# Performance work log

Measured on AMD Instinct MI355X. Metric: run time of the kernel, lower is better.

The kernel has to match this reference:

```python
import jax, jax.numpy as jnp
import numpy as np

B, H0, W0, C, NH, G = 2, 256, 256, 64, 4, 8
PD = (C // 4) // 4  # DynamicPosBias pos_dim = 4
HID = 4 * C


def _ln(x, g, b, eps=1e-5):
    mu = jnp.mean(x, -1, keepdims=True)
    var = jnp.mean((x - mu) ** 2, -1, keepdims=True)
    return (x - mu) * jax.lax.rsqrt(var + eps) * g + b


def setup_inputs():
    key = jax.random.key(0)
    ks = iter(jax.random.split(key, 48))
    w = lambda shape: jax.random.normal(next(ks), shape, jnp.float32) * 0.02
    return {
        'x': jax.random.normal(next(ks), (B, H0 * W0, C), jnp.float32),
        'y': jax.random.normal(next(ks), (B, H0 * W0, C), jnp.float32),
        'norm1_g': jnp.ones((C,), jnp.float32), 'norm1_b': jnp.zeros((C,), jnp.float32),
        'qkv_w': w((C, 3 * C)), 'qkv_b': jnp.zeros((3 * C,), jnp.float32),
        'proj_w': w((C, C)), 'proj_b': jnp.zeros((C,), jnp.float32),
        'pp_w': w((2, PD)), 'pp_b': jnp.zeros((PD,), jnp.float32),
        'ln1_g': jnp.ones((PD,), jnp.float32), 'ln1_b': jnp.zeros((PD,), jnp.float32),
        'l1_w': w((PD, PD)), 'l1_b': jnp.zeros((PD,), jnp.float32),
        'ln2_g': jnp.ones((PD,), jnp.float32), 'ln2_b': jnp.zeros((PD,), jnp.float32),
        'l2_w': w((PD, PD)), 'l2_b': jnp.zeros((PD,), jnp.float32),
        'ln3_g': jnp.ones((PD,), jnp.float32), 'ln3_b': jnp.zeros((PD,), jnp.float32),
        'l3_w': w((PD, NH)), 'l3_b': jnp.zeros((NH,), jnp.float32),
        'norm2_g': jnp.ones((C,), jnp.float32), 'norm2_b': jnp.zeros((C,), jnp.float32),
        'fx1_w': w((C, HID)), 'fx1_b': jnp.zeros((HID,), jnp.float32),
        'fx2_w': w((HID, C)), 'fx2_b': jnp.zeros((C,), jnp.float32),
        'fy1_w': w((C, HID)), 'fy1_b': jnp.zeros((HID,), jnp.float32),
        'fy2_w': w((HID, C)), 'fy2_b': jnp.zeros((C,), jnp.float32),
        'H': H0, 'W': W0,
    }


def reference(x, y, norm1_g, norm1_b, qkv_w, qkv_b, proj_w, proj_b,
              pp_w, pp_b, ln1_g, ln1_b, l1_w, l1_b, ln2_g, ln2_b, l2_w, l2_b,
              ln3_g, ln3_b, l3_w, l3_b, norm2_g, norm2_b,
              fx1_w, fx1_b, fx2_w, fx2_b, fy1_w, fy1_b, fy2_w, fy2_b, H, W):
    Bb, L, Cc = x.shape
    d = Cc // NH
    xn = _ln(x, norm1_g, norm1_b).reshape(Bb, H, W, Cc)
    yn = _ln(y, norm1_g, norm1_b).reshape(Bb, H, W, Cc)

    def part(t):  # (B,H,W,C) -> (B*nW, G*G, C)
        t = t.reshape(Bb, H // G, G, W // G, G, Cc).transpose(0, 1, 3, 2, 4, 5)
        return t.reshape(-1, G * G, Cc)

    # merge both modalities' patches of the same window along the token axis
    tok = tok = jnp.concatenate([part(xn), part(yn)], axis=1)  # (B_, 2*G*G, C)
    Gh, Gw = 2 * G, G
    N = Gh * Gw

    # dynamic relative position bias (small MLP + gather)
    bh = jnp.arange(1 - Gh, Gh)
    bw = jnp.arange(1 - Gw, Gw)
    biases = jnp.stack(jnp.meshgrid(bh, bw, indexing='ij'), 0).reshape(2, -1).T.astype(x.dtype)
    coords = jnp.stack(jnp.meshgrid(jnp.arange(Gh), jnp.arange(Gw), indexing='ij'), 0).reshape(2, -1)
    rel = (coords[:, :, None] - coords[:, None, :]).transpose(1, 2, 0)
    ridx = (rel[..., 0] + Gh - 1) * (2 * Gw - 1) + (rel[..., 1] + Gw - 1)  # (N,N)
    p = biases @ pp_w + pp_b
    p = jax.nn.relu(_ln(p, ln1_g, ln1_b)) @ l1_w + l1_b
    p = jax.nn.relu(_ln(p, ln2_g, ln2_b)) @ l2_w + l2_b
    p = jax.nn.relu(_ln(p, ln3_g, ln3_b)) @ l3_w + l3_b  # ((2Gh-1)*(2Gw-1), NH)
    rpb = p[ridx.reshape(-1)].reshape(N, N, NH).transpose(2, 0, 1)  # (NH,N,N)

    # windowed multi-head attention
    qkv = (tok @ qkv_w + qkv_b).reshape(-1, N, 3, NH, d).transpose(2, 0, 3, 1, 4)
    q, k, v = qkv[0] * (d ** -0.5), qkv[1], qkv[2]
    attn = jnp.einsum('bhnd,bhmd->bhnm', q, k) + rpb[None]
    attn = jax.nn.softmax(attn, axis=-1)
    out = jnp.einsum('bhnm,bhmd->bhnd', attn, v).transpose(0, 2, 1, 3).reshape(-1, N, Cc)
    out = out @ proj_w + proj_b

    def rev(t):  # (B*nW, G*G, C) -> (B, H*W, C)
        t = t.reshape(Bb, H // G, W // G, G, G, Cc).transpose(0, 1, 3, 2, 4, 5)
        return t.reshape(Bb, H * W, Cc)

    x = x + rev(out[:, :G * G])
    y = y + rev(out[:, G * G:])

    def mlp(t, w1, b1, w2, b2):
        return jax.nn.gelu(t @ w1 + b1, approximate=False) @ w2 + b2

    x = x + mlp(_ln(x, norm2_g, norm2_b), fx1_w, fx1_b, fx2_w, fx2_b)
    y = y + mlp(_ln(y, norm2_g, norm2_b), fy1_w, fy1_b, fy2_w, fy2_b)
    return x, y
```

## Files before the change

### kernel.cpp

```cpp
#include <hip/hip_runtime.h>
#include <math.h>

constexpr int CC    = 64;
constexpr int GG    = 8;
constexpr int H0    = 256;
constexpr int W0c   = 256;
constexpr int BB    = 2;
constexpr int LL    = H0 * W0c;
constexpr int NWIN  = BB * (H0 / GG) * (W0c / GG);
constexpr int HIDN  = 256;
constexpr int NBIA  = 31 * 15;
constexpr long long MODSZ = (long long)BB * LL * CC;

constexpr float INV_LN2 = 1.4426950408889634f;

constexpr int WS_PTAB  = 0;
constexpr int WS_BIAS  = 8192;
constexpr int WS_WQKV  = 270336;
constexpr int WS_WPROJ = 294912;
constexpr int WS_MLPW  = 303104;

using f32x4  = __attribute__((ext_vector_type(4))) float;
using bf16x8 = __attribute__((ext_vector_type(8))) short;
using bf16x4 = __attribute__((ext_vector_type(4))) short;

static __device__ __forceinline__ short to_bf16(float f) {
  unsigned u = __float_as_uint(f);
  unsigned r = (u + 0x7FFFu + ((u >> 16) & 1u)) >> 16;
  return (short)r;
}
static __device__ __forceinline__ bf16x4 mk4_bf16(float a, float b, float c, float d) {
  unsigned p0 = ((__float_as_uint(a) + 0x8000u) >> 16) | ((__float_as_uint(b) + 0x8000u) & 0xFFFF0000u);
  unsigned p1 = ((__float_as_uint(c) + 0x8000u) >> 16) | ((__float_as_uint(d) + 0x8000u) & 0xFFFF0000u);
  bf16x4 r;
  r[0] = (short)(p0 & 0xFFFFu); r[1] = (short)(p0 >> 16);
  r[2] = (short)(p1 & 0xFFFFu); r[3] = (short)(p1 >> 16);
  return r;
}
static __device__ __forceinline__ float gelu_tanh(float u) {
  float u2 = u * u;
  float t  = fmaf(0.044715f, u2, 1.0f);
  float z  = u * t * 1.5957691216057308f;
  float e  = __expf(-z);
  return u / (1.0f + e);
}

static __device__ __forceinline__ void ln4_relu(float* p, const float* g, const float* b) {
  float mu = 0.25f * (p[0] + p[1] + p[2] + p[3]);
  float d0 = p[0] - mu, d1 = p[1] - mu, d2 = p[2] - mu, d3 = p[3] - mu;
  float var = 0.25f * (d0 * d0 + d1 * d1 + d2 * d2 + d3 * d3);
  float rs = rsqrtf(var + 1e-5f);
  p[0] = fmaxf(d0 * rs * g[0] + b[0], 0.0f);
  p[1] = fmaxf(d1 * rs * g[1] + b[1], 0.0f);
  p[2] = fmaxf(d2 * rs * g[2] + b[2], 0.0f);
  p[3] = fmaxf(d3 * rs * g[3] + b[3], 0.0f);
}
static __device__ __forceinline__ void mm4(const float* a, const float* w, const float* b, float* o) {
  #pragma unroll
  for (int j = 0; j < 4; ++j) {
    float s = b[j];
    #pragma unroll
    for (int i = 0; i < 4; ++i) s += a[i] * w[i * 4 + j];
    o[j] = s;
  }
}

__global__ void pbias_kernel(const float* __restrict__ pp_w, const float* __restrict__ pp_b,
                             const float* __restrict__ ln1g, const float* __restrict__ ln1b,
                             const float* __restrict__ l1w,  const float* __restrict__ l1b,
                             const float* __restrict__ ln2g, const float* __restrict__ ln2b,
                             const float* __restrict__ l2w,  const float* __restrict__ l2b,
                             const float* __restrict__ ln3g, const float* __restrict__ ln3b,
                             const float* __restrict__ l3w,  const float* __restrict__ l3b,
                             float* __restrict__ p_table) {
  int r = blockIdx.x * blockDim.x + threadIdx.x;
  if (r >= NBIA) return;
  float bh = (float)(r / 15 - 15);
  float bw = (float)(r % 15 - 7);
  float a[4], t[4];
  #pragma unroll
  for (int j = 0; j < 4; ++j) a[j] = bh * pp_w[j] + bw * pp_w[4 + j] + pp_b[j];
  ln4_relu(a, ln1g, ln1b);
  mm4(a, l1w, l1b, t);
  ln4_relu(t, ln2g, ln2b);
  mm4(t, l2w, l2b, a);
  ln4_relu(a, ln3g, ln3b);
  mm4(a, l3w, l3b, t);
  #pragma unroll
  for (int j = 0; j < 4; ++j) p_table[r * 4 + j] = t[j];
}

__global__ void bias_expand_kernel(const float* __restrict__ p_table, float* __restrict__ bias_exp) {
  int gid = blockIdx.x * 256 + threadIdx.x;
  int h   = gid >> 12;
  int rem = gid & 4095;
  int q   = rem >> 5;
  int k0  = (rem & 31) * 4;
  int qih = q >> 3, qiw = q & 7;
  float o[4];
  #pragma unroll
  for (int kk = 0; kk < 4; ++kk) {
    int k = k0 + kk;
    int ridx = (qih - (k >> 3) + 15) * 15 + (qiw - (k & 7) + 7);
    o[kk] = p_table[ridx * 4 + h] * INV_LN2;
  }
  f32x4 v = {o[0], o[1], o[2], o[3]};
  *(f32x4*)(bias_exp + gid * 4) = v;
}

__global__ void prep_w_kernel(const float* __restrict__ qkv_w, const float* __restrict__ proj_w,
                              short* __restrict__ wqkvF, short* __restrict__ projF) {
  int t = blockIdx.x * 256 + threadIdx.x;
  if (t < 12288) {
    int slot = t >> 9, e = t & 511;
    int lp = e >> 3, j = e & 7;
    int ng = slot >> 1, s = slot & 1;
    int k   = 32 * s + 8 * (lp >> 4) + j;
    int col = 16 * ng + (lp & 15);
    float v = qkv_w[k * 192 + col];
    if (col < 64) v *= 0.25f * INV_LN2;
    wqkvF[t] = to_bf16(v);
  } else {
    int t2 = t - 12288;
    int slot = t2 >> 9, e = t2 & 511;
    int lp = e >> 3, j = e & 7;
    int ng = slot >> 1, s = slot & 1;
    int k   = 32 * s + 8 * (lp >> 4) + j;
    int col = 16 * ng + (lp & 15);
    projF[t2] = to_bf16(proj_w[k * 64 + col]);
  }
}

__global__ void prep_mlp_w_kernel(const float* __restrict__ fx1w, const float* __restrict__ fy1w,
                                  const float* __restrict__ fx2w, const float* __restrict__ fy2w,
                                  short* __restrict__ mlpW) {
  int gid = blockIdx.x * 256 + threadIdx.x;
  int img = gid >> 14;
  int e   = gid & 16383;
  int slot = e >> 9, lp = (e >> 3) & 63, j = e & 7;
  float v;
  if (img < 2) {
    const float* w1 = img ? fy1w : fx1w;
    int nt = slot >> 1, ks = slot & 1;
    int in_ch = ks * 32 + ((lp >> 4) << 3) + j;
    int hid   = nt * 16 + (lp & 15);
    v = w1[in_ch * HIDN + hid];
  } else {
    const float* w2 = (img & 1) ? fy2w : fx2w;
    int nt2 = slot >> 3, g2 = slot & 7;
    int hid = g2 * 32 + ((lp >> 4) << 3) + j;
    int oc  = nt2 * 16 + (lp & 15);
    v = w2[hid * CC + oc];
  }
  mlpW[gid] = to_bf16(v);
}

__launch_bounds__(256, 2)
__global__ void win_attn_kernel(const float* __restrict__ x, const float* __restrict__ y,
                                const float* __restrict__ n1g, const float* __restrict__ n1b,
                                const float* __restrict__ qkv_b, const float* __restrict__ proj_b,
                                const float* __restrict__ bias_exp,
                                const short* __restrict__ wqkvF, const short* __restrict__ projF,
                                float* __restrict__ out) {
  __shared__ __align__(16) char smem[81920];
  char* const TOK_ = smem;
  char* const QB_  = smem + 16384;
  char* const KB_  = smem + 32768;
  char* const VT_  = smem + 49152;
  char* const PB_  = smem + 65536;

  const int tid = threadIdx.x;
  const int l   = tid & 63;
  const int l15 = l & 15;
  const int lg  = l >> 4;
  const int wv  = __builtin_amdgcn_readfirstlane(tid >> 6);

  const int widx = blockIdx.x;
  const int b  = widx >> 10;
  const int wl = widx & 1023;
  const int wh = wl >> 5, ww = wl & 31;

  {
    const int lane16 = tid & 15;
    const float4 g4 = *(const float4*)(n1g + lane16 * 4);
    const float4 b4 = *(const float4*)(n1b + lane16 * 4);
    #pragma unroll
    for (int ps = 0; ps < 8; ++ps) {
      int t  = ps * 16 + (tid >> 4);
      int g  = t & 63;
      const float* src = ((t & 64) ? y : x)
          + ((long long)b * LL + (long long)(wh * GG + (g >> 3)) * W0c + (ww * GG + (g & 7))) * CC
          + lane16 * 4;
      float4 v = *(const float4*)src;
      float s  = v.x + v.y + v.z + v.w;
      float s2 = v.x * v.x + v.y * v.y + v.z * v.z + v.w * v.w;
      #pragma unroll
      for (int m = 1; m < 16; m <<= 1) { s += __shfl_xor(s, m); s2 += __shfl_xor(s2, m); }
      float mu  = s * (1.0f / 64.0f);
      float var = fmaxf(s2 * (1.0f / 64.0f) - mu * mu, 0.0f);
      float rs  = rsqrtf(var + 1e-5f);
      bf16x4 w4 = mk4_bf16((v.x - mu) * rs * g4.x + b4.x,
                           (v.y - mu) * rs * g4.y + b4.y,
                           (v.z - mu) * rs * g4.z + b4.z,
                           (v.w - mu) * rs * g4.w + b4.w);
      *(bf16x4*)(TOK_ + ((t * 128 + lane16 * 8) ^ ((t & 7) << 4))) = w4;
    }
  }
  __syncthreads();

  {
    bf16x8 awq[2][2];
    #pragma unroll
    for (int ct = 0; ct < 2; ++ct)
      #pragma unroll
      for (int ks = 0; ks < 2; ++ks)
        awq[ct][ks] = *(const bf16x8*)((const char*)wqkvF + ((((2 * wv + ct) * 2 + ks)) << 10) + l * 16);
    bf16x8 bwv[2];
    #pragma unroll
    for (int ks = 0; ks < 2; ++ks)
      bwv[ks] = *(const bf16x8*)((const char*)wqkvF + (((8 + wv) * 2 + ks) << 10) + l * 16);

    f32x4 bq[2];
    #pragma unroll
    for (int ct = 0; ct < 2; ++ct) {
      f32x4 bb = *(const f32x4*)(qkv_b + (2 * wv + ct) * 16 + lg * 4);
      if (wv < 2) {
        const float qs = 0.25f * INV_LN2;
        bb[0] *= qs; bb[1] *= qs; bb[2] *= qs; bb[3] *= qs;
      }
      bq[ct] = bb;
    }
    const float bv = qkv_b[128 + wv * 16 + l15];
    char* const QKbuf = (wv < 2) ? QB_ : KB_;
    const int chv = wv * 16 + l15;
    const int vswz = (chv & 7) << 4;

    #pragma unroll
    for (int nt = 0; nt < 8; ++nt) {
      const int row = 16 * nt + l15;
      const int rswz = (row & 7) << 4;
      bf16x8 t0 = *(const bf16x8*)(TOK_ + ((row * 128 +  0 + lg * 16) ^ rswz));
      bf16x8 t1 = *(const bf16x8*)(TOK_ + ((row * 128 + 64 + lg * 16) ^ rswz));
      #pragma unroll
      for (int ct = 0; ct < 2; ++ct) {
        f32x4 a = bq[ct];
        a = __builtin_amdgcn_mfma_f32_16x16x32_bf16(awq[ct][0], t0, a, 0, 0, 0);
        a = __builtin_amdgcn_mfma_f32_16x16x32_bf16(awq[ct][1], t1, a, 0, 0, 0);
        int chL = (((2 * wv + ct) * 16) & 63) + lg * 4;
        *(bf16x4*)(QKbuf + ((row * 128 + chL * 2) ^ rswz)) = mk4_bf16(a[0], a[1], a[2], a[3]);
      }
      {
        f32x4 a = {bv, bv, bv, bv};
        a = __builtin_amdgcn_mfma_f32_16x16x32_bf16(t0, bwv[0], a, 0, 0, 0);
        a = __builtin_amdgcn_mfma_f32_16x16x32_bf16(t1, bwv[1], a, 0, 0, 0);
        int tok0 = 16 * nt + lg * 4;
        *(bf16x4*)(VT_ + ((chv * 256 + tok0 * 2) ^ vswz)) = mk4_bf16(a[0], a[1], a[2], a[3]);
      }
    }
  }
  __syncthreads();

  {
    const int h = wv;
    const float* biasH = bias_exp + h * 16384;
    bf16x8 kf[8];
    #pragma unroll
    for (int kt = 0; kt < 8; ++kt) {
      bf16x8 f = {0, 0, 0, 0, 0, 0, 0, 0};
      if (l < 32) {
        int row = 16 * kt + l15;
        f = *(const bf16x8*)(KB_ + ((row * 128 + h * 32 + lg * 16) ^ ((row & 7) << 4)));
      }
      kf[kt] = f;
    }
    bf16x8 vf[4];
    #pragma unroll
    for (int ks = 0; ks < 4; ++ks) {
      int row = h * 16 + l15;
      vf[ks] = *(const bf16x8*)(VT_ + ((row * 256 + ks * 64 + lg * 16) ^ ((row & 7) << 4)));
    }
    char* const PBw = PB_ + wv * 4096;
    const int pswz = (l15 & 7) << 4;

    for (int qt = 0; qt < 8; ++qt) {
      f32x4 bias[8];
      #pragma unroll
      for (int kt = 0; kt < 8; ++kt)
        bias[kt] = *(const f32x4*)(biasH + (16 * qt + l15) * 128 + 16 * kt + 4 * lg);
      bf16x8 qf = {0, 0, 0, 0, 0, 0, 0, 0};
      if (l < 32) {
        int row = 16 * qt + l15;
        qf = *(const bf16x8*)(QB_ + ((row * 128 + h * 32 + lg * 16) ^ ((row & 7) << 4)));
      }
      f32x4 s[8];
      #pragma unroll
      for (int kt = 0; kt < 8; ++kt)
        s[kt] = __builtin_amdgcn_mfma_f32_16x16x32_bf16(kf[kt], qf, bias[kt], 0, 0, 0);
      float sum = 0.0f;
      #pragma unroll
      for (int kt = 0; kt < 8; ++kt) {
        s[kt][0] = __builtin_amdgcn_exp2f(s[kt][0]);
        s[kt][1] = __builtin_amdgcn_exp2f(s[kt][1]);
        s[kt][2] = __builtin_amdgcn_exp2f(s[kt][2]);
        s[kt][3] = __builtin_amdgcn_exp2f(s[kt][3]);
        sum += (s[kt][0] + s[kt][1]) + (s[kt][2] + s[kt][3]);
      }
      sum += __shfl_xor(sum, 16);
      sum += __shfl_xor(sum, 32);
      float inv = 1.0f / sum;
      #pragma unroll
      for (int kt = 0; kt < 8; ++kt) {
        int k0 = 16 * kt + 4 * lg;
        *(bf16x4*)(PBw + ((l15 * 256 + k0 * 2) ^ pswz)) = mk4_bf16(s[kt][0], s[kt][1], s[kt][2], s[kt][3]);
      }
      f32x4 pacc = {0.0f, 0.0f, 0.0f, 0.0f};
      #pragma unroll
      for (int ks = 0; ks < 4; ++ks) {
        bf16x8 pa = *(const bf16x8*)(PBw + ((l15 * 256 + ks * 64 + lg * 16) ^ pswz));
        pacc = __builtin_amdgcn_mfma_f32_16x16x32_bf16(vf[ks], pa, pacc, 0, 0, 0);
      }
      pacc[0] *= inv; pacc[1] *= inv; pacc[2] *= inv; pacc[3] *= inv;
      *(bf16x4*)(TOK_ + (((16 * qt + l15) * 128 + (h * 16 + lg * 4) * 2) ^ (((16 * qt + l15) & 7) << 4)))
          = mk4_bf16(pacc[0], pacc[1], pacc[2], pacc[3]);
    }
  }
  __syncthreads();

  {
    bf16x8 pa2[2];
    #pragma unroll
    for (int ks = 0; ks < 2; ++ks)
      pa2[ks] = *(const bf16x8*)((const char*)projF + (((wv * 2 + ks)) << 10) + l * 16);
    const f32x4 bp = *(const f32x4*)(proj_b + wv * 16 + lg * 4);
    #pragma unroll
    for (int nt = 0; nt < 8; ++nt) {
      const int row = 16 * nt + l15;
      const int rswz = (row & 7) << 4;
      bf16x8 t0 = *(const bf16x8*)(TOK_ + ((row * 128 +  0 + lg * 16) ^ rswz));
      bf16x8 t1 = *(const bf16x8*)(TOK_ + ((row * 128 + 64 + lg * 16) ^ rswz));
      f32x4 acc = bp;
      acc = __builtin_amdgcn_mfma_f32_16x16x32_bf16(pa2[0], t0, acc, 0, 0, 0);
      acc = __builtin_amdgcn_mfma_f32_16x16x32_bf16(pa2[1], t1, acc, 0, 0, 0);
      int g = row & 63;
      long long base = ((long long)b * LL + (long long)(wh * GG + (g >> 3)) * W0c + (ww * GG + (g & 7))) * CC
                       + wv * 16 + lg * 4;
      const float* src = ((row & 64) ? y : x) + base;
      float* dst = out + ((row & 64) ? MODSZ : 0) + base;
      f32x4 sv = *(const f32x4*)src;
      sv[0] += acc[0]; sv[1] += acc[1]; sv[2] += acc[2]; sv[3] += acc[3];
      *(f32x4*)dst = sv;
    }
  }
}

__launch_bounds__(256, 3)
__global__ void mlp_mfma_kernel(const float* __restrict__ n2g, const float* __restrict__ n2b,
                                const float* __restrict__ fx1b, const float* __restrict__ fx2b,
                                const float* __restrict__ fy1b, const float* __restrict__ fy2b,
                                const short* __restrict__ mlpW, float* __restrict__ out) {
  __shared__ __align__(16) char AR4[4][8192];

  const int tid = threadIdx.x;
  const int l   = tid & 63;
  const int l15 = l & 15;
  const int lg  = l >> 4;
  const int wv  = tid >> 6;
  const int bid = blockIdx.x;
  const int mod = bid >> 10;
  const long long wtok0 = (long long)(bid & 1023) * 128 + wv * 32;

  const float* b1 = mod ? fy1b : fx1b;
  const float* b2 = mod ? fy2b : fx2b;
  const short* w1T = mlpW + mod * 16384;
  const short* w2T = mlpW + 32768 + mod * 16384;
  float* const outm = out + (long long)mod * MODSZ;

  char* const TOKw = AR4[wv];
  char* const HBw  = AR4[wv] + 4608;

  {
    const f32x4 g4 = *(const f32x4*)(n2g + l15 * 4);
    const f32x4 b4 = *(const f32x4*)(n2b + l15 * 4);
    #pragma unroll
    for (int ps = 0; ps < 8; ++ps) {
      int t = ps * 4 + lg;
      const float* rp = outm + (wtok0 + t) * CC + l15 * 4;
      f32x4 v = *(const f32x4*)rp;
      float s  = v[0] + v[1] + v[2] + v[3];
      float s2 = v[0] * v[0] + v[1] * v[1] + v[2] * v[2] + v[3] * v[3];
      #pragma unroll
      for (int m = 1; m < 16; m <<= 1) { s += __shfl_xor(s, m); s2 += __shfl_xor(s2, m); }
      float mu  = s * (1.0f / 64.0f);
      float var = fmaxf(s2 * (1.0f / 64.0f) - mu * mu, 0.0f);
      float rs  = rsqrtf(var + 1e-5f);
      bf16x4 w4 = mk4_bf16((v[0] - mu) * rs * g4[0] + b4[0],
                           (v[1] - mu) * rs * g4[1] + b4[1],
                           (v[2] - mu) * rs * g4[2] + b4[2],
                           (v[3] - mu) * rs * g4[3] + b4[3]);
      *(bf16x4*)(TOKw + t * 144 + l15 * 8) = w4;
    }
  }

  bf16x8 tokB[2][2];
  #pragma unroll
  for (int ct = 0; ct < 2; ++ct)
    #pragma unroll
    for (int ks = 0; ks < 2; ++ks)
      tokB[ct][ks] = *(const bf16x8*)(TOKw + (16 * ct + l15) * 144 + ks * 64 + lg * 16);

  f32x4 acc2[4][2];
  #pragma unroll
  for (int n = 0; n < 4; ++n) {
    f32x4 bb = *(const f32x4*)(b2 + n * 16 + lg * 4);
    acc2[n][0] = bb; acc2[n][1] = bb;
  }

  #pragma unroll 1
  for (int g2 = 0; g2 < 8; ++g2) {
    #pragma unroll
    for (int sub = 0; sub < 2; ++sub) {
      const int nt = g2 * 2 + sub;
      bf16x8 wa0 = *(const bf16x8*)(w1T + ((nt * 2 + 0) << 9) + l * 8);
      bf16x8 wa1 = *(const bf16x8*)(w1T + ((nt * 2 + 1) << 9) + l * 8);
      f32x4 z = {0.0f, 0.0f, 0.0f, 0.0f};
      f32x4 d0 = __builtin_amdgcn_mfma_f32_16x16x32_bf16(wa0, tokB[0][0], z, 0, 0, 0);
      d0 = __builtin_amdgcn_mfma_f32_16x16x32_bf16(wa1, tokB[0][1], d0, 0, 0, 0);
      f32x4 d1 = __builtin_amdgcn_mfma_f32_16x16x32_bf16(wa0, tokB[1][0], z, 0, 0, 0);
      d1 = __builtin_amdgcn_mfma_f32_16x16x32_bf16(wa1, tokB[1][1], d1, 0, 0, 0);
      f32x4 b1v = *(const f32x4*)(b1 + nt * 16 + lg * 4);
      bf16x4 h0 = mk4_bf16(gelu_tanh(d0[0] + b1v[0]), gelu_tanh(d0[1] + b1v[1]),
                           gelu_tanh(d0[2] + b1v[2]), gelu_tanh(d0[3] + b1v[3]));
      bf16x4 h1 = mk4_bf16(gelu_tanh(d1[0] + b1v[0]), gelu_tanh(d1[1] + b1v[1]),
                           gelu_tanh(d1[2] + b1v[2]), gelu_tanh(d1[3] + b1v[3]));
      *(bf16x4*)(HBw + l15 * 80        + sub * 32 + lg * 8) = h0;
      *(bf16x4*)(HBw + (16 + l15) * 80 + sub * 32 + lg * 8) = h1;
    }
    bf16x8 hb0 = *(const bf16x8*)(HBw + l15 * 80        + lg * 16);
    bf16x8 hb1 = *(const bf16x8*)(HBw + (16 + l15) * 80 + lg * 16);
    #pragma unroll
    for (int n = 0; n < 4; ++n) {
      bf16x8 wa = *(const bf16x8*)(w2T + ((n * 8 + g2) << 9) + l * 8);
      acc2[n][0] = __builtin_amdgcn_mfma_f32_16x16x32_bf16(wa, hb0, acc2[n][0], 0, 0, 0);
      acc2[n][1] = __builtin_amdgcn_mfma_f32_16x16x32_bf16(wa, hb1, acc2[n][1], 0, 0, 0);
    }
  }

  #pragma unroll
  for (int n = 0; n < 4; ++n)
    #pragma unroll
    for (int ct = 0; ct < 2; ++ct) {
      float* rp = outm + (wtok0 + 16 * ct + l15) * CC + n * 16 + lg * 4;
      f32x4 o = *(const f32x4*)rp;
      o[0] += acc2[n][ct][0]; o[1] += acc2[n][ct][1];
      o[2] += acc2[n][ct][2]; o[3] += acc2[n][ct][3];
      *(f32x4*)rp = o;
    }
}

extern "C" void kernel_launch(void* const* d_in, const int* in_sizes, int n_in,
                              void* d_out, int out_size, void* d_ws, size_t ws_size,
                              hipStream_t stream) {
  const float* x      = (const float*)d_in[0];
  const float* y      = (const float*)d_in[1];
  const float* n1g    = (const float*)d_in[2];
  const float* n1b    = (const float*)d_in[3];
  const float* qkv_w  = (const float*)d_in[4];
  const float* qkv_b  = (const float*)d_in[5];
  const float* proj_w = (const float*)d_in[6];
  const float* proj_b = (const float*)d_in[7];
  const float* pp_w   = (const float*)d_in[8];
  const float* pp_b   = (const float*)d_in[9];
  const float* ln1g   = (const float*)d_in[10];
  const float* ln1b   = (const float*)d_in[11];
  const float* l1w    = (const float*)d_in[12];
  const float* l1b    = (const float*)d_in[13];
  const float* ln2g   = (const float*)d_in[14];
  const float* ln2b   = (const float*)d_in[15];
  const float* l2w    = (const float*)d_in[16];
  const float* l2b    = (const float*)d_in[17];
  const float* ln3g   = (const float*)d_in[18];
  const float* ln3b   = (const float*)d_in[19];
  const float* l3w    = (const float*)d_in[20];
  const float* l3b    = (const float*)d_in[21];
  const float* n2g    = (const float*)d_in[22];
  const float* n2b    = (const float*)d_in[23];
  const float* fx1w   = (const float*)d_in[24];
  const float* fx1b   = (const float*)d_in[25];
  const float* fx2w   = (const float*)d_in[26];
  const float* fx2b   = (const float*)d_in[27];
  const float* fy1w   = (const float*)d_in[28];
  const float* fy1b   = (const float*)d_in[29];
  const float* fy2w   = (const float*)d_in[30];
  const float* fy2b   = (const float*)d_in[31];
  (void)in_sizes; (void)n_in; (void)out_size; (void)ws_size;

  float* out = (float*)d_out;
  char*  ws  = (char*)d_ws;
  float* p_table  = (float*)(ws + WS_PTAB);
  float* bias_exp = (float*)(ws + WS_BIAS);
  short* wqkvF    = (short*)(ws + WS_WQKV);
  short* projF    = (short*)(ws + WS_WPROJ);
  short* mlpW     = (short*)(ws + WS_MLPW);

  pbias_kernel<<<1, 512, 0, stream>>>(pp_w, pp_b, ln1g, ln1b, l1w, l1b,
                                      ln2g, ln2b, l2w, l2b, ln3g, ln3b, l3w, l3b, p_table);
  bias_expand_kernel<<<64, 256, 0, stream>>>(p_table, bias_exp);
  prep_w_kernel<<<64, 256, 0, stream>>>(qkv_w, proj_w, wqkvF, projF);
  prep_mlp_w_kernel<<<256, 256, 0, stream>>>(fx1w, fy1w, fx2w, fy2w, mlpW);
  win_attn_kernel<<<NWIN, 256, 0, stream>>>(x, y, n1g, n1b, qkv_b, proj_b,
                                            bias_exp, wqkvF, projF, out);
  mlp_mfma_kernel<<<2048, 256, 0, stream>>>(n2g, n2b, fx1b, fx2b, fy1b, fy2b,
                                            mlpW, out);
}
```

Baseline: 169.4 us.

## Keep per-head Q/K/V in registers and redistribute via shuffles instead of LDS

Each wave now computes Q, K and V for its own head and keeps them packed as bf16 in registers. The MFMA operand fragments are rebuilt with cross-lane shuffles instead of being written to and reread from shared-memory staging buffers. This cuts the LDS footprint from 80KB to 32KB and raises the launch bound to 4 blocks per SM, aiming for higher occupancy and less LDS traffic. In exchange it adds many shuffle instructions and register pressure under the tighter occupancy target. The bias loads also move inside the MFMA loop rather than being prefetched up front.

```diff
diff --git a/kernel.cpp b/kernel.cpp
--- a/kernel.cpp
+++ b/kernel.cpp
@@ -23,6 +23,7 @@
 using f32x4  = __attribute__((ext_vector_type(4))) float;
 using bf16x8 = __attribute__((ext_vector_type(8))) short;
 using bf16x4 = __attribute__((ext_vector_type(4))) short;
+using u32x2  = __attribute__((ext_vector_type(2))) unsigned;
 
 static __device__ __forceinline__ short to_bf16(float f) {
   unsigned u = __float_as_uint(f);
@@ -36,6 +37,36 @@
   r[0] = (short)(p0 & 0xFFFFu); r[1] = (short)(p0 >> 16);
   r[2] = (short)(p1 & 0xFFFFu); r[3] = (short)(p1 >> 16);
   return r;
+}
+static __device__ __forceinline__ u32x2 pk2_bf16(float a, float b, float c, float d) {
+  u32x2 r;
+  r[0] = ((__float_as_uint(a) + 0x8000u) >> 16) | ((__float_as_uint(b) + 0x8000u) & 0xFFFF0000u);
+  r[1] = ((__float_as_uint(c) + 0x8000u) >> 16) | ((__float_as_uint(d) + 0x8000u) & 0xFFFF0000u);
+  return r;
+}
+static __device__ __forceinline__ bf16x8 frag_from(u32x2 pk, int srcA, bool valid) {
+  int a0 = __shfl((int)pk[0], srcA);
+  int a1 = __shfl((int)pk[1], srcA);
+  int b0 = __shfl((int)pk[0], srcA + 16);
+  int b1 = __shfl((int)pk[1], srcA + 16);
+  union { int i[4]; bf16x8 v; } u;
+  u.i[0] = valid ? a0 : 0;
+  u.i[1] = valid ? a1 : 0;
+  u.i[2] = valid ? b0 : 0;
+  u.i[3] = valid ? b1 : 0;
+  return u.v;
+}
+static __device__ __forceinline__ bf16x8 frag_from2(u32x2 pkLo, u32x2 pkHi, int srcA, bool useHi) {
+  int a0l = __shfl((int)pkLo[0], srcA);      int a0h = __shfl((int)pkHi[0], srcA);
+  int a1l = __shfl((int)pkLo[1], srcA);      int a1h = __shfl((int)pkHi[1], srcA);
+  int b0l = __shfl((int)pkLo[0], srcA + 16); int b0h = __shfl((int)pkHi[0], srcA + 16);
+  int b1l = __shfl((int)pkLo[1], srcA + 16); int b1h = __shfl((int)pkHi[1], srcA + 16);
+  union { int i[4]; bf16x8 v; } u;
+  u.i[0] = useHi ? a0h : a0l;
+  u.i[1] = useHi ? a1h : a1l;
+  u.i[2] = useHi ? b0h : b0l;
+  u.i[3] = useHi ? b1h : b1l;
+  return u.v;
 }
 static __device__ __forceinline__ float gelu_tanh(float u) {
   float u2 = u * u;
@@ -155,19 +186,16 @@
   mlpW[gid] = to_bf16(v);
 }
 
-__launch_bounds__(256, 2)
+__launch_bounds__(256, 4)
 __global__ void win_attn_kernel(const float* __restrict__ x, const float* __restrict__ y,
                                 const float* __restrict__ n1g, const float* __restrict__ n1b,
                                 const float* __restrict__ qkv_b, const float* __restrict__ proj_b,
                                 const float* __restrict__ bias_exp,
                                 const short* __restrict__ wqkvF, const short* __restrict__ projF,
                                 float* __restrict__ out) {
-  __shared__ __align__(16) char smem[81920];
+  __shared__ __align__(16) char smem[32768];
   char* const TOK_ = smem;
-  char* const QB_  = smem + 16384;
-  char* const KB_  = smem + 32768;
-  char* const VT_  = smem + 49152;
-  char* const PB_  = smem + 65536;
+  char* const PB_  = smem + 16384;
 
   const int tid = threadIdx.x;
   const int l   = tid & 63;
@@ -208,32 +236,20 @@
   }
   __syncthreads();
 
+  u32x2 Qpk[8], Kpk[8], Vpk[8];
   {
-    bf16x8 awq[2][2];
-    #pragma unroll
-    for (int ct = 0; ct < 2; ++ct)
-      #pragma unroll
-      for (int ks = 0; ks < 2; ++ks)
-        awq[ct][ks] = *(const bf16x8*)((const char*)wqkvF + ((((2 * wv + ct) * 2 + ks)) << 10) + l * 16);
-    bf16x8 bwv[2];
-    #pragma unroll
-    for (int ks = 0; ks < 2; ++ks)
-      bwv[ks] = *(const bf16x8*)((const char*)wqkvF + (((8 + wv) * 2 + ks) << 10) + l * 16);
-
-    f32x4 bq[2];
-    #pragma unroll
-    for (int ct = 0; ct < 2; ++ct) {
-      f32x4 bb = *(const f32x4*)(qkv_b + (2 * wv + ct) * 16 + lg * 4);
-      if (wv < 2) {
-        const float qs = 0.25f * INV_LN2;
-        bb[0] *= qs; bb[1] *= qs; bb[2] *= qs; bb[3] *= qs;
-      }
-      bq[ct] = bb;
-    }
-    const float bv = qkv_b[128 + wv * 16 + l15];
-    char* const QKbuf = (wv < 2) ? QB_ : KB_;
-    const int chv = wv * 16 + l15;
-    const int vswz = (chv & 7) << 4;
+    const int h = wv;
+    bf16x8 aq0 = *(const bf16x8*)((const char*)wqkvF + ((2 * h + 0) << 10) + l * 16);
+    bf16x8 aq1 = *(const bf16x8*)((const char*)wqkvF + ((2 * h + 1) << 10) + l * 16);
+    bf16x8 ak0 = *(const bf16x8*)((const char*)wqkvF + ((8 + 2 * h + 0) << 10) + l * 16);
+    bf16x8 ak1 = *(const bf16x8*)((const char*)wqkvF + ((8 + 2 * h + 1) << 10) + l * 16);
+    bf16x8 bv0 = *(const bf16x8*)((const char*)wqkvF + ((16 + 2 * h + 0) << 10) + l * 16);
+    bf16x8 bv1 = *(const bf16x8*)((const char*)wqkvF + ((16 + 2 * h + 1) << 10) + l * 16);
+    f32x4 bqQ = *(const f32x4*)(qkv_b + 16 * h + lg * 4);
+    const float qs = 0.25f * INV_LN2;
+    bqQ[0] *= qs; bqQ[1] *= qs; bqQ[2] *= qs; bqQ[3] *= qs;
+    const f32x4 bqK = *(const f32x4*)(qkv_b + 64 + 16 * h + lg * 4);
+    const float bvv = qkv_b[128 + 16 * h + l15];
 
     #pragma unroll
     for (int nt = 0; nt < 8; ++nt) {
@@ -241,21 +257,16 @@
       const int rswz = (row & 7) << 4;
       bf16x8 t0 = *(const bf16x8*)(TOK_ + ((row * 128 +  0 + lg * 16) ^ rswz));
       bf16x8 t1 = *(const bf16x8*)(TOK_ + ((row * 128 + 64 + lg * 16) ^ rswz));
-      #pragma unroll
-      for (int ct = 0; ct < 2; ++ct) {
-        f32x4 a = bq[ct];
-        a = __builtin_amdgcn_mfma_f32_16x16x32_bf16(awq[ct][0], t0, a, 0, 0, 0);
-        a = __builtin_amdgcn_mfma_f32_16x16x32_bf16(awq[ct][1], t1, a, 0, 0, 0);
-        int chL = (((2 * wv + ct) * 16) & 63) + lg * 4;
-        *(bf16x4*)(QKbuf + ((row * 128 + chL * 2) ^ rswz)) = mk4_bf16(a[0], a[1], a[2], a[3]);
-      }
-      {
-        f32x4 a = {bv, bv, bv, bv};
-        a = __builtin_amdgcn_mfma_f32_16x16x32_bf16(t0, bwv[0], a, 0, 0, 0);
-        a = __builtin_amdgcn_mfma_f32_16x16x32_bf16(t1, bwv[1], a, 0, 0, 0);
-        int tok0 = 16 * nt + lg * 4;
-        *(bf16x4*)(VT_ + ((chv * 256 + tok0 * 2) ^ vswz)) = mk4_bf16(a[0], a[1], a[2], a[3]);
-      }
+      f32x4 dq = __builtin_amdgcn_mfma_f32_16x16x32_bf16(aq0, t0, bqQ, 0, 0, 0);
+      dq = __builtin_amdgcn_mfma_f32_16x16x32_bf16(aq1, t1, dq, 0, 0, 0);
+      f32x4 dk = __builtin_amdgcn_mfma_f32_16x16x32_bf16(ak0, t0, bqK, 0, 0, 0);
+      dk = __builtin_amdgcn_mfma_f32_16x16x32_bf16(ak1, t1, dk, 0, 0, 0);
+      f32x4 dv = {bvv, bvv, bvv, bvv};
+      dv = __builtin_amdgcn_mfma_f32_16x16x32_bf16(t0, bv0, dv, 0, 0, 0);
+      dv = __builtin_amdgcn_mfma_f32_16x16x32_bf16(t1, bv1, dv, 0, 0, 0);
+      Qpk[nt] = pk2_bf16(dq[0], dq[1], dq[2], dq[3]);
+      Kpk[nt] = pk2_bf16(dk[0], dk[1], dk[2], dk[3]);
+      Vpk[nt] = pk2_bf16(dv[0], dv[1], dv[2], dv[3]);
     }
   }
   __syncthreads();
@@ -263,39 +274,25 @@
   {
     const int h = wv;
     const float* biasH = bias_exp + h * 16384;
+    const int srcA = l15 + 32 * (lg & 1);
+    const bool lowHalf = (lg < 2);
     bf16x8 kf[8];
     #pragma unroll
-    for (int kt = 0; kt < 8; ++kt) {
-      bf16x8 f = {0, 0, 0, 0, 0, 0, 0, 0};
-      if (l < 32) {
-        int row = 16 * kt + l15;
-        f = *(const bf16x8*)(KB_ + ((row * 128 + h * 32 + lg * 16) ^ ((row & 7) << 4)));
-      }
-      kf[kt] = f;
-    }
+    for (int kt = 0; kt < 8; ++kt) kf[kt] = frag_from(Kpk[kt], srcA, lowHalf);
     bf16x8 vf[4];
     #pragma unroll
-    for (int ks = 0; ks < 4; ++ks) {
-      int row = h * 16 + l15;
-      vf[ks] = *(const bf16x8*)(VT_ + ((row * 256 + ks * 64 + lg * 16) ^ ((row & 7) << 4)));
-    }
+    for (int ks = 0; ks < 4; ++ks) vf[ks] = frag_from2(Vpk[2 * ks], Vpk[2 * ks + 1], srcA, lg >= 2);
     char* const PBw = PB_ + wv * 4096;
     const int pswz = (l15 & 7) << 4;
 
     for (int qt = 0; qt < 8; ++qt) {
-      f32x4 bias[8];
-      #pragma unroll
-      for (int kt = 0; kt < 8; ++kt)
-        bias[kt] = *(const f32x4*)(biasH + (16 * qt + l15) * 128 + 16 * kt + 4 * lg);
-      bf16x8 qf = {0, 0, 0, 0, 0, 0, 0, 0};
-      if (l < 32) {
-        int row = 16 * qt + l15;
-        qf = *(const bf16x8*)(QB_ + ((row * 128 + h * 32 + lg * 16) ^ ((row & 7) << 4)));
-      }
+      bf16x8 qf = frag_from(Qpk[qt], srcA, lowHalf);
       f32x4 s[8];
       #pragma unroll
-      for (int kt = 0; kt < 8; ++kt)
-        s[kt] = __builtin_amdgcn_mfma_f32_16x16x32_bf16(kf[kt], qf, bias[kt], 0, 0, 0);
+      for (int kt = 0; kt < 8; ++kt) {
+        f32x4 bias = *(const f32x4*)(biasH + (16 * qt + l15) * 128 + 16 * kt + 4 * lg);
+        s[kt] = __builtin_amdgcn_mfma_f32_16x16x32_bf16(kf[kt], qf, bias, 0, 0, 0);
+      }
       float sum = 0.0f;
       #pragma unroll
       for (int kt = 0; kt < 8; ++kt) {
```

New measurement: 176.7 us. 4.3% more time.
